# Kernel optimization log

Hardware: AMD Instinct MI355X
Metric: run time of the kernel (lower is better)

## Reference

```python
import jax, jax.numpy as jnp
import numpy as np

BATCH = 16384
IN_F = 768
OUT_F = 768
GRID_SIZE = 8           # act_fun.get_size()
GRID_LO, GRID_HI = -2.0, 2.0


def rbf_basis(x):
    """Gaussian RBF spline basis: [b, i] -> [b, a, i]."""
    grid = jnp.linspace(GRID_LO, GRID_HI, GRID_SIZE, dtype=x.dtype)  # [a]
    h = (GRID_HI - GRID_LO) / (GRID_SIZE - 1)
    z = (x[:, None, :] - grid[None, :, None]) / h                    # [b, a, i]
    return jnp.exp(-z * z)


def setup_inputs() -> dict:
    key = jax.random.key(0)
    k1, k2, k3 = jax.random.split(key, 3)
    x = jax.random.normal(k1, (BATCH, IN_F), dtype=jnp.float32)
    # xavier_normal_(gain=0.001): std = 0.001 * sqrt(2 / (fan_in + fan_out))
    std_wb = 0.001 * np.sqrt(2.0 / (IN_F + OUT_F))
    w_b = jax.random.normal(k2, (OUT_F, IN_F), dtype=jnp.float32) * std_wb
    w_s = jnp.ones((OUT_F, IN_F), dtype=jnp.float32)
    c = jax.random.normal(k3, (GRID_SIZE, OUT_F, IN_F), dtype=jnp.float32) * 0.001
    return {"x": x, "w_b": w_b, "w_s": w_s, "c": c}


def reference(x, w_b, w_s, c):
    # Original: sum_i[ (sum_a phi(x)_{bai} c_{aoi}) * w_s_{oi} + silu(x)_{bi} * w_b_{oi} ]
    phi = rbf_basis(x)                       # [b, a, i]
    cw = c * w_s[None, :, :]                 # fold scale into coeffs: [a, o, i]
    spline = jnp.einsum('bai,aoi->bo', phi, cw)   # fused contraction over (a, i)
    res = jax.nn.silu(x) @ w_b.T             # [b, o]
    return spline + res
```

## Files before the change

kernel.cpp:

```cpp
#include <hip/hip_runtime.h>
#include <hip/hip_bf16.h>

#define BATCH 16384
#define INF 768
#define OUTF 768
#define NSLAB 9
#define KTOT (NSLAB * INF)
#define BM 128
#define BN 128
#define BK 64
#define KB_TILES (INF / BK)
#define NIT (NSLAB * KB_TILES)

#define LOG2E 1.4426950408889634f
#define EXPM2 0.13533528323661270f

typedef __bf16 bf16x8 __attribute__((ext_vector_type(8)));
typedef float f32x4 __attribute__((ext_vector_type(4)));
typedef unsigned short ushort8v __attribute__((ext_vector_type(8)));

__device__ __forceinline__ unsigned short f2bf(float f) {
  unsigned u = __builtin_bit_cast(unsigned, f);
  u += 0x7fffu + ((u >> 16) & 1u);
  return (unsigned short)(u >> 16);
}

__device__ __forceinline__ unsigned cvt2(float a, float b) {
  __hip_bfloat162 h = __float22bfloat162_rn(make_float2(a, b));
  unsigned r;
  __builtin_memcpy(&r, &h, 4);
  return r;
}

__device__ __forceinline__ bf16x8 pack8(const f32x4 a, const f32x4 b) {
  union { uint4 u; bf16x8 v; } r;
  r.u.x = cvt2(a[0], a[1]); r.u.y = cvt2(a[2], a[3]);
  r.u.z = cvt2(b[0], b[1]); r.u.w = cvt2(b[2], b[3]);
  return r.v;
}

__device__ __forceinline__ void gload_lds16(const void* g, void* l) {
  __builtin_amdgcn_global_load_lds(
      (const __attribute__((address_space(1))) unsigned int*)g,
      (__attribute__((address_space(3))) unsigned int*)l, 16, 0, 0);
}

__global__ __launch_bounds__(256) void build_bext(
    const float* __restrict__ w_b, const float* __restrict__ w_s,
    const float* __restrict__ c, unsigned short* __restrict__ bext) {
  const int tid = blockIdx.x * 256 + threadIdx.x;
  const int o = tid / (KTOT / 8);
  const int k = (tid - o * (KTOT / 8)) * 8;
  const int a = k / INF;
  const int i = k - a * INF;
  float4 v0, v1;
  if (a < 8) {
    const float* cp = c + ((size_t)(a * OUTF + o)) * INF + i;
    const float* wp = w_s + (size_t)o * INF + i;
    const float4 c0 = *(const float4*)cp, c1 = *(const float4*)(cp + 4);
    const float4 s0 = *(const float4*)wp, s1 = *(const float4*)(wp + 4);
    v0 = make_float4(c0.x * s0.x, c0.y * s0.y, c0.z * s0.z, c0.w * s0.w);
    v1 = make_float4(c1.x * s1.x, c1.y * s1.y, c1.z * s1.z, c1.w * s1.w);
  } else {
    const float* bp = w_b + (size_t)o * INF + i;
    v0 = *(const float4*)bp;
    v1 = *(const float4*)(bp + 4);
  }
  ushort8v r;
  r[0] = f2bf(v0.x); r[1] = f2bf(v0.y); r[2] = f2bf(v0.z); r[3] = f2bf(v0.w);
  r[4] = f2bf(v1.x); r[5] = f2bf(v1.y); r[6] = f2bf(v1.z); r[7] = f2bf(v1.w);
  *(ushort8v*)(bext + (size_t)o * KTOT + k) = r;
}

__global__ __launch_bounds__(256, 2) void kan_gemm5(
    const float* __restrict__ x, const unsigned short* __restrict__ bext,
    float* __restrict__ out) {
  __shared__ unsigned short Bs[4][BN * BK];

  const int orig = blockIdx.x;
  const int bid = (orig & 7) * 96 + (orig >> 3);
  const int cb = bid / (BATCH / BM);
  const int rb = bid - cb * (BATCH / BM);
  const int row0 = rb * BM, col0 = cb * BN;

  const int t = threadIdx.x;
  const int lane = t & 63;
  const int w = t >> 6;
  const int lrow = lane & 15, lhi = lane >> 4;
  const int rgrp = lane >> 3, ch = lane & 7;

  f32x4 acc[2][8];
#pragma unroll
  for (int mt = 0; mt < 2; ++mt)
#pragma unroll
    for (int n = 0; n < 8; ++n)
      acc[mt][n] = (f32x4){0.f, 0.f, 0.f, 0.f};

  const unsigned short* gB0 =
      bext + (size_t)(col0 + w * 32 + rgrp) * KTOT + (size_t)(ch ^ rgrp) * 8;

  auto kt_of = [&](int k) {
    const int ib = k / 9;
    const int r = k - ib * 9;
    const int s = (r == 0) ? 8 : (r - 1);
    return s * KB_TILES + ib;
  };

  auto stage_b = [&](int k) {
    const unsigned short* gB = gB0 + (size_t)kt_of(k) * BK;
    unsigned short* l = &Bs[k & 3][w * 2048];
#pragma unroll
    for (int q = 0; q < 4; ++q)
      gload_lds16(gB + (size_t)q * 8 * KTOT, l + q * 512);
  };

  const float* xr0 = x + (size_t)(row0 + w * 32 + lrow) * INF;
  const float* xr1 = xr0 + 16 * INF;

  f32x4 ph[2][2][2], gg[2][2][2];
  f32x4 xn[2][2][2];

  auto load_x = [&](int ib) {
#pragma unroll
    for (int mt = 0; mt < 2; ++mt)
#pragma unroll
      for (int kk = 0; kk < 2; ++kk) {
        const float* p = (mt ? xr1 : xr0) + ib * BK + kk * 32 + lhi * 8;
        xn[mt][kk][0] = *(const f32x4*)p;
        xn[mt][kk][1] = *(const f32x4*)(p + 4);
      }
  };

  load_x(0);
  stage_b(0);
  stage_b(1);
  stage_b(2);
  asm volatile("s_waitcnt vmcnt(8)" ::: "memory");
  __builtin_amdgcn_s_barrier();
  __builtin_amdgcn_sched_barrier(0);

  int s_c = 8, ib_c = 0;
  for (int it = 0; it < NIT; ++it) {
    const int cur = it & 3;
    const bool xpf = (s_c == 6) && (ib_c + 1 < KB_TILES);
    if (xpf) load_x(ib_c + 1);
    if (it + 3 < NIT) stage_b(it + 3);

    bf16x8 af[2][2];
    if (s_c == 8) {
#pragma unroll
      for (int mt = 0; mt < 2; ++mt)
#pragma unroll
        for (int kk = 0; kk < 2; ++kk) {
          const f32x4 x0 = xn[mt][kk][0], x1 = xn[mt][kk][1];
          f32x4 s0, s1;
#pragma unroll
          for (int e = 0; e < 4; ++e) {
            s0[e] = x0[e] * __builtin_amdgcn_rcpf(
                        1.f + __builtin_amdgcn_exp2f(x0[e] * (-LOG2E)));
            s1[e] = x1[e] * __builtin_amdgcn_rcpf(
                        1.f + __builtin_amdgcn_exp2f(x1[e] * (-LOG2E)));
          }
          af[mt][kk] = pack8(s0, s1);
          const f32x4 z0 = x0 * 1.75f + 3.5f;
          const f32x4 z1 = x1 * 1.75f + 3.5f;
#pragma unroll
          for (int e = 0; e < 4; ++e) {
            ph[mt][kk][0][e] = __builtin_amdgcn_exp2f(-(z0[e] * z0[e]) * LOG2E);
            ph[mt][kk][1][e] = __builtin_amdgcn_exp2f(-(z1[e] * z1[e]) * LOG2E);
            gg[mt][kk][0][e] = __builtin_amdgcn_exp2f(z0[e] * (2.f * LOG2E) - LOG2E);
            gg[mt][kk][1][e] = __builtin_amdgcn_exp2f(z1[e] * (2.f * LOG2E) - LOG2E);
          }
        }
    } else {
#pragma unroll
      for (int mt = 0; mt < 2; ++mt)
#pragma unroll
        for (int kk = 0; kk < 2; ++kk) {
          af[mt][kk] = pack8(ph[mt][kk][0], ph[mt][kk][1]);
          ph[mt][kk][0] *= gg[mt][kk][0];
          ph[mt][kk][1] *= gg[mt][kk][1];
          gg[mt][kk][0] = gg[mt][kk][0] * EXPM2;
          gg[mt][kk][1] = gg[mt][kk][1] * EXPM2;
        }
    }

#pragma unroll
    for (int kk = 0; kk < 2; ++kk) {
      bf16x8 bfr[8];
#pragma unroll
      for (int n = 0; n < 8; ++n) {
        const int rowB = n * 16 + lrow;
        const int chB = (kk * 4 + lhi) ^ (lrow & 7);
        bfr[n] = *(const bf16x8*)&Bs[cur][rowB * 64 + chB * 8];
      }
#pragma unroll
      for (int mt = 0; mt < 2; ++mt)
#pragma unroll
        for (int n = 0; n < 8; ++n)
          acc[mt][n] = __builtin_amdgcn_mfma_f32_16x16x32_bf16(
              af[mt][kk], bfr[n], acc[mt][n], 0, 0, 0);
    }

    if (it < NIT - 3) {
      if (xpf) asm volatile("s_waitcnt vmcnt(16)" ::: "memory");
      else     asm volatile("s_waitcnt vmcnt(8)" ::: "memory");
    } else if (it == NIT - 3) {
      asm volatile("s_waitcnt vmcnt(4)" ::: "memory");
    } else if (it == NIT - 2) {
      asm volatile("s_waitcnt vmcnt(0)" ::: "memory");
    }
    if (it < NIT - 1) {
      __builtin_amdgcn_s_barrier();
      __builtin_amdgcn_sched_barrier(0);
    }

    if (s_c == 8)      { s_c = 0; }
    else if (s_c == 7) { s_c = 8; ib_c++; }
    else               { s_c++; }
  }

#pragma unroll
  for (int mt = 0; mt < 2; ++mt) {
#pragma unroll
    for (int n = 0; n < 8; ++n) {
      const int row = row0 + w * 32 + mt * 16 + lhi * 4;
      const int col = col0 + n * 16 + lrow;
#pragma unroll
      for (int r = 0; r < 4; ++r)
        out[(size_t)(row + r) * OUTF + col] = acc[mt][n][r];
    }
  }
}

#define PK (BK + 8)
__device__ __forceinline__ float phi_f(float x, float g) {
  float z = (x - g) * 1.75f;
  return __expf(-z * z);
}
__device__ __forceinline__ float silu_f(float x) {
  return x / (1.f + __expf(-x));
}

__global__ __launch_bounds__(256, 2) void kan_gemm_fb(
    const float* __restrict__ x, const float* __restrict__ w_b,
    const float* __restrict__ w_s, const float* __restrict__ c,
    float* __restrict__ out) {
  __shared__ unsigned short As[BM][PK];
  __shared__ unsigned short Bs[BN][PK];

  const int bid = blockIdx.x;
  const int cb = bid % (OUTF / BN);
  const int rb = bid / (OUTF / BN);
  const int row0 = rb * BM, col0 = cb * BN;

  const int t = threadIdx.x;
  const int lane = t & 63;
  const int w = t >> 6;
  const int wr = w >> 1, wc = w & 1;
  const int lrow = lane & 15, lhi = lane >> 4;

  f32x4 acc[4][4];
#pragma unroll
  for (int m = 0; m < 4; ++m)
#pragma unroll
    for (int n = 0; n < 4; ++n)
      acc[m][n] = (f32x4){0.f, 0.f, 0.f, 0.f};

  const int rsub = t >> 4;
  const int k4 = t & 15;

  for (int kt = 0; kt < KTOT / BK; ++kt) {
    const int a = kt / KB_TILES;
    const int i0 = (kt % KB_TILES) * BK;
    const float ga = -2.f + (float)a * (4.f / 7.f);

#pragma unroll
    for (int p = 0; p < 8; ++p) {
      const int r = p * 16 + rsub;
      const float4 xv = *(const float4*)(x + (size_t)(row0 + r) * INF + i0 + k4 * 4);
      ushort4 av;
      if (a < 8) {
        av.x = f2bf(phi_f(xv.x, ga)); av.y = f2bf(phi_f(xv.y, ga));
        av.z = f2bf(phi_f(xv.z, ga)); av.w = f2bf(phi_f(xv.w, ga));
      } else {
        av.x = f2bf(silu_f(xv.x)); av.y = f2bf(silu_f(xv.y));
        av.z = f2bf(silu_f(xv.z)); av.w = f2bf(silu_f(xv.w));
      }
      *(ushort4*)&As[r][k4 * 4] = av;

      ushort4 bv;
      if (a < 8) {
        const float4 cv = *(const float4*)(c + ((size_t)a * OUTF + col0 + r) * INF + i0 + k4 * 4);
        const float4 wv = *(const float4*)(w_s + (size_t)(col0 + r) * INF + i0 + k4 * 4);
        bv.x = f2bf(cv.x * wv.x); bv.y = f2bf(cv.y * wv.y);
        bv.z = f2bf(cv.z * wv.z); bv.w = f2bf(cv.w * wv.w);
      } else {
        const float4 bbv = *(const float4*)(w_b + (size_t)(col0 + r) * INF + i0 + k4 * 4);
        bv.x = f2bf(bbv.x); bv.y = f2bf(bbv.y);
        bv.z = f2bf(bbv.z); bv.w = f2bf(bbv.w);
      }
      *(ushort4*)&Bs[r][k4 * 4] = bv;
    }
    __syncthreads();

#pragma unroll
    for (int kk = 0; kk < 2; ++kk) {
      bf16x8 af[4], bfr[4];
#pragma unroll
      for (int m = 0; m < 4; ++m)
        af[m] = *(const bf16x8*)&As[wr * 64 + m * 16 + lrow][kk * 32 + lhi * 8];
#pragma unroll
      for (int n = 0; n < 4; ++n)
        bfr[n] = *(const bf16x8*)&Bs[wc * 64 + n * 16 + lrow][kk * 32 + lhi * 8];
#pragma unroll
      for (int m = 0; m < 4; ++m)
#pragma unroll
        for (int n = 0; n < 4; ++n)
          acc[m][n] = __builtin_amdgcn_mfma_f32_16x16x32_bf16(af[m], bfr[n], acc[m][n], 0, 0, 0);
    }
    __syncthreads();
  }

#pragma unroll
  for (int m = 0; m < 4; ++m) {
#pragma unroll
    for (int n = 0; n < 4; ++n) {
      const int row = row0 + wr * 64 + m * 16 + lhi * 4;
      const int col = col0 + wc * 64 + n * 16 + lrow;
#pragma unroll
      for (int r = 0; r < 4; ++r)
        out[(size_t)(row + r) * OUTF + col] = acc[m][n][r];
    }
  }
}

extern "C" void kernel_launch(void* const* d_in, const int* in_sizes, int n_in,
                              void* d_out, int out_size, void* d_ws, size_t ws_size,
                              hipStream_t stream) {
  const float* x   = (const float*)d_in[0];
  const float* w_b = (const float*)d_in[1];
  const float* w_s = (const float*)d_in[2];
  const float* c   = (const float*)d_in[3];
  float* out = (float*)d_out;

  const size_t need = (size_t)OUTF * KTOT * sizeof(unsigned short);
  if (ws_size >= need) {
    unsigned short* bext = (unsigned short*)d_ws;
    build_bext<<<(OUTF * KTOT / 8) / 256, 256, 0, stream>>>(w_b, w_s, c, bext);
    kan_gemm5<<<(BATCH / BM) * (OUTF / BN), 256, 0, stream>>>(x, bext, out);
  } else {
    kan_gemm_fb<<<(BATCH / BM) * (OUTF / BN), 256, 0, stream>>>(x, w_b, w_s, c, out);
  }
}
```

Baseline: 246.6 us.

## Retile KAN GEMM to 64x128x32 blocks with column-split warps

Shrinks the block tile to 64 rows by 128 columns with a K step of 32, and reassigns warps so each owns 32 output columns across all 64 rows. The B staging, swizzle, x prefetch and waitcnt schedule are adjusted to match, and the block-index remap is updated for the doubled grid. The intent is more blocks and smaller per-iteration work for better latency hiding and balance. The cost is that every warp recomputes the RBF/SiLU basis for the same rows, and twice as many barrier-separated iterations run with fewer MFMAs each.

```diff
diff --git a/kernel.cpp b/kernel.cpp
--- a/kernel.cpp
+++ b/kernel.cpp
@@ -6,9 +6,9 @@
 #define OUTF 768
 #define NSLAB 9
 #define KTOT (NSLAB * INF)
-#define BM 128
+#define BM 64
 #define BN 128
-#define BK 64
+#define BK 32
 #define KB_TILES (INF / BK)
 #define NIT (NSLAB * KB_TILES)
 
@@ -72,13 +72,13 @@
   *(ushort8v*)(bext + (size_t)o * KTOT + k) = r;
 }
 
-__global__ __launch_bounds__(256, 2) void kan_gemm5(
+__global__ __launch_bounds__(256, 2) void kan_gemm6(
     const float* __restrict__ x, const unsigned short* __restrict__ bext,
     float* __restrict__ out) {
   __shared__ unsigned short Bs[4][BN * BK];
 
   const int orig = blockIdx.x;
-  const int bid = (orig & 7) * 96 + (orig >> 3);
+  const int bid = (orig & 7) * 192 + (orig >> 3);
   const int cb = bid / (BATCH / BM);
   const int rb = bid - cb * (BATCH / BM);
   const int row0 = rb * BM, col0 = cb * BN;
@@ -87,128 +87,108 @@
   const int lane = t & 63;
   const int w = t >> 6;
   const int lrow = lane & 15, lhi = lane >> 4;
-  const int rgrp = lane >> 3, ch = lane & 7;
-
-  f32x4 acc[2][8];
-#pragma unroll
-  for (int mt = 0; mt < 2; ++mt)
-#pragma unroll
-    for (int n = 0; n < 8; ++n)
+
+  f32x4 acc[4][2];
+#pragma unroll
+  for (int mt = 0; mt < 4; ++mt)
+#pragma unroll
+    for (int n = 0; n < 2; ++n)
       acc[mt][n] = (f32x4){0.f, 0.f, 0.f, 0.f};
 
-  const unsigned short* gB0 =
-      bext + (size_t)(col0 + w * 32 + rgrp) * KTOT + (size_t)(ch ^ rgrp) * 8;
-
-  auto kt_of = [&](int k) {
-    const int ib = k / 9;
-    const int r = k - ib * 9;
-    const int s = (r == 0) ? 8 : (r - 1);
-    return s * KB_TILES + ib;
+  const int srow = t >> 2;
+  const int sch = (t & 3) ^ (srow & 3);
+  const unsigned short* gS0 = bext + (size_t)(col0 + srow) * KTOT + sch * 8;
+  const unsigned short* gS1 = gS0 + (size_t)64 * KTOT;
+
+  auto stage_b = [&](int k) {
+    const int ib = k / 9, r = k - ib * 9;
+    const int kt = (r ? r - 1 : 8) * KB_TILES + ib;
+    unsigned short* l = &Bs[k & 3][t * 8];
+    gload_lds16(gS0 + (size_t)kt * BK, l);
+    gload_lds16(gS1 + (size_t)kt * BK, l + 2048);
   };
 
-  auto stage_b = [&](int k) {
-    const unsigned short* gB = gB0 + (size_t)kt_of(k) * BK;
-    unsigned short* l = &Bs[k & 3][w * 2048];
-#pragma unroll
-    for (int q = 0; q < 4; ++q)
-      gload_lds16(gB + (size_t)q * 8 * KTOT, l + q * 512);
-  };
-
-  const float* xr0 = x + (size_t)(row0 + w * 32 + lrow) * INF;
-  const float* xr1 = xr0 + 16 * INF;
-
-  f32x4 ph[2][2][2], gg[2][2][2];
-  f32x4 xn[2][2][2];
+  f32x4 ph[4][2], gg[4][2];
+  f32x4 xn[4][2];
 
   auto load_x = [&](int ib) {
 #pragma unroll
-    for (int mt = 0; mt < 2; ++mt)
-#pragma unroll
-      for (int kk = 0; kk < 2; ++kk) {
-        const float* p = (mt ? xr1 : xr0) + ib * BK + kk * 32 + lhi * 8;
-        xn[mt][kk][0] = *(const f32x4*)p;
-        xn[mt][kk][1] = *(const f32x4*)(p + 4);
-      }
+    for (int mt = 0; mt < 4; ++mt) {
+      const float* p = x + (size_t)(row0 + mt * 16 + lrow) * INF + ib * BK + lhi * 8;
+      xn[mt][0] = *(const f32x4*)p;
+      xn[mt][1] = *(const f32x4*)(p + 4);
+    }
   };
 
   load_x(0);
   stage_b(0);
   stage_b(1);
   stage_b(2);
-  asm volatile("s_waitcnt vmcnt(8)" ::: "memory");
+  asm volatile("s_waitcnt vmcnt(4)" ::: "memory");
   __builtin_amdgcn_s_barrier();
   __builtin_amdgcn_sched_barrier(0);
 
   int s_c = 8, ib_c = 0;
   for (int it = 0; it < NIT; ++it) {
     const int cur = it & 3;
-    const bool xpf = (s_c == 6) && (ib_c + 1 < KB_TILES);
+    const bool xpf = (s_c == 7) && (ib_c + 1 < KB_TILES);
     if (xpf) load_x(ib_c + 1);
     if (it + 3 < NIT) stage_b(it + 3);
 
-    bf16x8 af[2][2];
+    bf16x8 af[4];
     if (s_c == 8) {
 #pragma unroll
-      for (int mt = 0; mt < 2; ++mt)
-#pragma unroll
-        for (int kk = 0; kk < 2; ++kk) {
-          const f32x4 x0 = xn[mt][kk][0], x1 = xn[mt][kk][1];
-          f32x4 s0, s1;
-#pragma unroll
-          for (int e = 0; e < 4; ++e) {
-            s0[e] = x0[e] * __builtin_amdgcn_rcpf(
-                        1.f + __builtin_amdgcn_exp2f(x0[e] * (-LOG2E)));
-            s1[e] = x1[e] * __builtin_amdgcn_rcpf(
-                        1.f + __builtin_amdgcn_exp2f(x1[e] * (-LOG2E)));
-          }
-          af[mt][kk] = pack8(s0, s1);
-          const f32x4 z0 = x0 * 1.75f + 3.5f;
-          const f32x4 z1 = x1 * 1.75f + 3.5f;
-#pragma unroll
-          for (int e = 0; e < 4; ++e) {
-            ph[mt][kk][0][e] = __builtin_amdgcn_exp2f(-(z0[e] * z0[e]) * LOG2E);
-            ph[mt][kk][1][e] = __builtin_amdgcn_exp2f(-(z1[e] * z1[e]) * LOG2E);
-            gg[mt][kk][0][e] = __builtin_amdgcn_exp2f(z0[e] * (2.f * LOG2E) - LOG2E);
-            gg[mt][kk][1][e] = __builtin_amdgcn_exp2f(z1[e] * (2.f * LOG2E) - LOG2E);
-          }
+      for (int mt = 0; mt < 4; ++mt) {
+        const f32x4 x0 = xn[mt][0], x1 = xn[mt][1];
+        f32x4 s0, s1;
+#pragma unroll
+        for (int e = 0; e < 4; ++e) {
+          s0[e] = x0[e] * __builtin_amdgcn_rcpf(
+                      1.f + __builtin_amdgcn_exp2f(x0[e] * (-LOG2E)));
+          s1[e] = x1[e] * __builtin_amdgcn_rcpf(
+                      1.f + __builtin_amdgcn_exp2f(x1[e] * (-LOG2E)));
         }
+        af[mt] = pack8(s0, s1);
+        const f32x4 z0 = x0 * 1.75f + 3.5f;
+        const f32x4 z1 = x1 * 1.75f + 3.5f;
+#pragma unroll
+        for (int e = 0; e < 4; ++e) {
+          ph[mt][0][e] = __builtin_amdgcn_exp2f(-(z0[e] * z0[e]) * LOG2E);
+          ph[mt][1][e] = __builtin_amdgcn_exp2f(-(z1[e] * z1[e]) * LOG2E);
+          gg[mt][0][e] = __builtin_amdgcn_exp2f(z0[e] * (2.f * LOG2E) - LOG2E);
+          gg[mt][1][e] = __builtin_amdgcn_exp2f(z1[e] * (2.f * LOG2E) - LOG2E);
+        }
+      }
     } else {
 #pragma unroll
-      for (int mt = 0; mt < 2; ++mt)
-#pragma unroll
-        for (int kk = 0; kk < 2; ++kk) {
-          af[mt][kk] = pack8(ph[mt][kk][0], ph[mt][kk][1]);
-          ph[mt][kk][0] *= gg[mt][kk][0];
-          ph[mt][kk][1] *= gg[mt][kk][1];
-          gg[mt][kk][0] = gg[mt][kk][0] * EXPM2;
-          gg[mt][kk][1] = gg[mt][kk][1] * EXPM2;
-        }
-    }
-
-#pragma unroll
-    for (int kk = 0; kk < 2; ++kk) {
-      bf16x8 bfr[8];
-#pragma unroll
-      for (int n = 0; n < 8; ++n) {
-        const int rowB = n * 16 + lrow;
-        const int chB = (kk * 4 + lhi) ^ (lrow & 7);
-        bfr[n] = *(const bf16x8*)&Bs[cur][rowB * 64 + chB * 8];
+      for (int mt = 0; mt < 4; ++mt) {
+        af[mt] = pack8(ph[mt][0], ph[mt][1]);
+        ph[mt][0] *= gg[mt][0];
+        ph[mt][1] *= gg[mt][1];
+        gg[mt][0] = gg[mt][0] * EXPM2;
+        gg[mt][1] = gg[mt][1] * EXPM2;
       }
-#pragma unroll
-      for (int mt = 0; mt < 2; ++mt)
-#pragma unroll
-        for (int n = 0; n < 8; ++n)
-          acc[mt][n] = __builtin_amdgcn_mfma_f32_16x16x32_bf16(
-              af[mt][kk], bfr[n], acc[mt][n], 0, 0, 0);
-    }
-
-    if (it < NIT - 3) {
-      if (xpf) asm volatile("s_waitcnt vmcnt(16)" ::: "memory");
-      else     asm volatile("s_waitcnt vmcnt(8)" ::: "memory");
+    }
+
+    bf16x8 bfr[2];
+    const int chB = lhi ^ (lrow & 3);
+#pragma unroll
+    for (int n = 0; n < 2; ++n)
+      bfr[n] = *(const bf16x8*)&Bs[cur][(w * 32 + n * 16 + lrow) * 32 + chB * 8];
+#pragma unroll
+    for (int mt = 0; mt < 4; ++mt)
+#pragma unroll
+      for (int n = 0; n < 2; ++n)
+        acc[mt][n] = __builtin_amdgcn_mfma_f32_16x16x32_bf16(
+            af[mt], bfr[n], acc[mt][n], 0, 0, 0);
+
+    if (it == NIT - 2) {
+      asm volatile("s_waitcnt vmcnt(0)" ::: "memory");
     } else if (it == NIT - 3) {
-      asm volatile("s_waitcnt vmcnt(4)" ::: "memory");
-    } else if (it == NIT - 2) {
-      asm volatile("s_waitcnt vmcnt(0)" ::: "memory");
+      asm volatile("s_waitcnt vmcnt(2)" ::: "memory");
+    } else if (it < NIT - 3) {
+      if (xpf) asm volatile("s_waitcnt vmcnt(2)" ::: "memory");
+      else     asm volatile("s_waitcnt vmcnt(4)" ::: "memory");
     }
     if (it < NIT - 1) {
       __builtin_amdgcn_s_barrier();
@@ -221,11 +201,11 @@
   }
 
 #pragma unroll
-  for (int mt = 0; mt < 2; ++mt) {
-#pragma unroll
-    for (int n = 0; n < 8; ++n) {
-      const int row = row0 + w * 32 + mt * 16 + lhi * 4;
-      const int col = col0 + n * 16 + lrow;
+  for (int mt = 0; mt < 4; ++mt) {
+#pragma unroll
+    for (int n = 0; n < 2; ++n) {
+      const int row = row0 + mt * 16 + lhi * 4;
+      const int col = col0 + w * 32 + n * 16 + lrow;
 #pragma unroll
       for (int r = 0; r < 4; ++r)
         out[(size_t)(row + r) * OUTF + col] = acc[mt][n][r];
@@ -233,7 +213,6 @@
   }
 }
 
-#define PK (BK + 8)
 __device__ __forceinline__ float phi_f(float x, float g) {
   float z = (x - g) * 1.75f;
   return __expf(-z * z);
@@ -246,13 +225,13 @@
     const float* __restrict__ x, const float* __restrict__ w_b,
     const float* __restrict__ w_s, const float* __restrict__ c,
     float* __restrict__ out) {
-  __shared__ unsigned short As[BM][PK];
-  __shared__ unsigned short Bs[BN][PK];
+  __shared__ unsigned short As[128][72];
+  __shared__ unsigned short Bs[128][72];
 
   const int bid = blockIdx.x;
-  const int cb = bid % (OUTF / BN);
-  const int rb = bid / (OUTF / BN);
-  const int row0 = rb * BM, col0 = cb * BN;
+  const int cb = bid % (OUTF / 128);
+  const int rb = bid / (OUTF / 128);
+  const int row0 = rb * 128, col0 = cb * 128;
 
   const int t = threadIdx.x;
   const int lane = t & 63;
@@ -270,9 +249,9 @@
   const int rsub = t >> 4;
   const int k4 = t & 15;
 
-  for (int kt = 0; kt < KTOT / BK; ++kt) {
-    const int a = kt / KB_TILES;
-    const int i0 = (kt % KB_TILES) * BK;
+  for (int kt = 0; kt < KTOT / 64; ++kt) {
+    const int a = kt / (INF / 64);
+    const int i0 = (kt % (INF / 64)) * 64;
     const float ga = -2.f + (float)a * (4.f / 7.f);
 
 #pragma unroll
@@ -348,8 +327,8 @@
   if (ws_size >= need) {
     unsigned short* bext = (unsigned short*)d_ws;
     build_bext<<<(OUTF * KTOT / 8) / 256, 256, 0, stream>>>(w_b, w_s, c, bext);
-    kan_gemm5<<<(BATCH / BM) * (OUTF / BN), 256, 0, stream>>>(x, bext, out);
+    kan_gemm6<<<(BATCH / BM) * (OUTF / BN), 256, 0, stream>>>(x, bext, out);
   } else {
-    kan_gemm_fb<<<(BATCH / BM) * (OUTF / BN), 256, 0, stream>>>(x, w_b, w_s, c, out);
-  }
-}
+    kan_gemm_fb<<<(BATCH / 128) * (OUTF / 128), 256, 0, stream>>>(x, w_b, w_s, c, out);
+  }
+}
```

Measured after the change: 604.4 us. +145.1%, slower.

## Pre-tile B into contiguous swizzled tiles and triple-buffer with 3 blocks/CU

Applied to the files above, without the earlier changes.

The weight-prep kernel now writes B in a tile-contiguous, pre-swizzled order so each stage is a straight contiguous copy into LDS instead of strided row reads. The main GEMM drops from four to three LDS buffers so three blocks fit per CU, and the loop is restructured as 12 outer input tiles by 9 unrolled slab steps with x loaded directly at slab start instead of prefetched. Fewer buffers mean a shorter prefetch distance and more exposed latency, and the register cap at 3 blocks/CU may force spills.

```diff
diff --git a/kernel.cpp b/kernel.cpp
--- a/kernel.cpp
+++ b/kernel.cpp
@@ -9,11 +9,15 @@
 #define BM 128
 #define BN 128
 #define BK 64
-#define KB_TILES (INF / BK)
-#define NIT (NSLAB * KB_TILES)
+#define KB_TILES 12
+#define NTILES (NSLAB * KB_TILES)
 
 #define LOG2E 1.4426950408889634f
 #define EXPM2 0.13533528323661270f
+
+#define TILE_SH 8192
+#define IB_SH   8192
+#define SLAB_SH (KB_TILES * TILE_SH)
 
 typedef __bf16 bf16x8 __attribute__((ext_vector_type(8)));
 typedef float f32x4 __attribute__((ext_vector_type(4)));
@@ -45,14 +49,22 @@
       (__attribute__((address_space(3))) unsigned int*)l, 16, 0, 0);
 }
 
-__global__ __launch_bounds__(256) void build_bext(
+__global__ __launch_bounds__(256) void build_bext2(
     const float* __restrict__ w_b, const float* __restrict__ w_s,
-    const float* __restrict__ c, unsigned short* __restrict__ bext) {
-  const int tid = blockIdx.x * 256 + threadIdx.x;
-  const int o = tid / (KTOT / 8);
-  const int k = (tid - o * (KTOT / 8)) * 8;
-  const int a = k / INF;
-  const int i = k - a * INF;
+    const float* __restrict__ c, unsigned short* __restrict__ bt) {
+  const int gid = blockIdx.x * 256 + threadIdx.x;
+  const int lane = gid & 63;
+  const int q = (gid >> 6) & 3;
+  const int wv = (gid >> 8) & 3;
+  const int tile = gid >> 10;
+  const int kt = tile % NTILES;
+  const int cbq = tile / NTILES;
+  const int a = kt / KB_TILES;
+  const int ib = kt - a * KB_TILES;
+  const int rg = lane >> 3, chh = lane & 7;
+  const int o = cbq * 128 + wv * 32 + q * 8 + rg;
+  const int i = ib * 64 + (chh ^ rg) * 8;
+
   float4 v0, v1;
   if (a < 8) {
     const float* cp = c + ((size_t)(a * OUTF + o)) * INF + i;
@@ -69,13 +81,13 @@
   ushort8v r;
   r[0] = f2bf(v0.x); r[1] = f2bf(v0.y); r[2] = f2bf(v0.z); r[3] = f2bf(v0.w);
   r[4] = f2bf(v1.x); r[5] = f2bf(v1.y); r[6] = f2bf(v1.z); r[7] = f2bf(v1.w);
-  *(ushort8v*)(bext + (size_t)o * KTOT + k) = r;
-}
-
-__global__ __launch_bounds__(256, 2) void kan_gemm5(
-    const float* __restrict__ x, const unsigned short* __restrict__ bext,
+  *(ushort8v*)(bt + (size_t)gid * 8) = r;
+}
+
+__global__ __launch_bounds__(256, 3) void kan_gemm7(
+    const float* __restrict__ x, const unsigned short* __restrict__ bt,
     float* __restrict__ out) {
-  __shared__ unsigned short Bs[4][BN * BK];
+  __shared__ unsigned short Bs[3][BN * BK];
 
   const int orig = blockIdx.x;
   const int bid = (orig & 7) * 96 + (orig >> 3);
@@ -87,7 +99,6 @@
   const int lane = t & 63;
   const int w = t >> 6;
   const int lrow = lane & 15, lhi = lane >> 4;
-  const int rgrp = lane >> 3, ch = lane & 7;
 
   f32x4 acc[2][8];
 #pragma unroll
@@ -96,128 +107,117 @@
     for (int n = 0; n < 8; ++n)
       acc[mt][n] = (f32x4){0.f, 0.f, 0.f, 0.f};
 
-  const unsigned short* gB0 =
-      bext + (size_t)(col0 + w * 32 + rgrp) * KTOT + (size_t)(ch ^ rgrp) * 8;
-
-  auto kt_of = [&](int k) {
-    const int ib = k / 9;
-    const int r = k - ib * 9;
-    const int s = (r == 0) ? 8 : (r - 1);
-    return s * KB_TILES + ib;
+  const unsigned short* gt =
+      bt + (size_t)cb * NTILES * TILE_SH + w * 2048 + lane * 8;
+  const float* xb = x + (size_t)(row0 + w * 32 + lrow) * INF;
+
+  const int c0 = lhi ^ (lrow & 7);
+  const int c1 = (4 + lhi) ^ (lrow & 7);
+  const unsigned short* pB0 = &Bs[0][lrow * 64 + c0 * 8];
+  const unsigned short* pB1 = &Bs[0][lrow * 64 + c1 * 8];
+
+  f32x4 ph[2][2][2], gg[2][2][2];
+
+  auto stage = [&](const unsigned short* src, int slot) {
+#pragma unroll
+    for (int q = 0; q < 4; ++q)
+      gload_lds16(src + q * 512, &Bs[slot][w * 2048 + q * 512]);
   };
 
-  auto stage_b = [&](int k) {
-    const unsigned short* gB = gB0 + (size_t)kt_of(k) * BK;
-    unsigned short* l = &Bs[k & 3][w * 2048];
-#pragma unroll
-    for (int q = 0; q < 4; ++q)
-      gload_lds16(gB + (size_t)q * 8 * KTOT, l + q * 512);
+  auto mma_kk = [&](int kk, int slot, bf16x8 af0, bf16x8 af1) {
+    const unsigned short* pB = kk ? pB1 : pB0;
+#pragma unroll
+    for (int n = 0; n < 8; ++n) {
+      const bf16x8 b = *(const bf16x8*)(pB + slot * TILE_SH + n * 1024);
+      acc[0][n] = __builtin_amdgcn_mfma_f32_16x16x32_bf16(af0, b, acc[0][n], 0, 0, 0);
+      acc[1][n] = __builtin_amdgcn_mfma_f32_16x16x32_bf16(af1, b, acc[1][n], 0, 0, 0);
+    }
   };
 
-  const float* xr0 = x + (size_t)(row0 + w * 32 + lrow) * INF;
-  const float* xr1 = xr0 + 16 * INF;
-
-  f32x4 ph[2][2][2], gg[2][2][2];
-  f32x4 xn[2][2][2];
-
-  auto load_x = [&](int ib) {
-#pragma unroll
-    for (int mt = 0; mt < 2; ++mt)
-#pragma unroll
-      for (int kk = 0; kk < 2; ++kk) {
-        const float* p = (mt ? xr1 : xr0) + ib * BK + kk * 32 + lhi * 8;
-        xn[mt][kk][0] = *(const f32x4*)p;
-        xn[mt][kk][1] = *(const f32x4*)(p + 4);
-      }
-  };
-
-  load_x(0);
-  stage_b(0);
-  stage_b(1);
-  stage_b(2);
-  asm volatile("s_waitcnt vmcnt(8)" ::: "memory");
+  const unsigned short* gib = gt;
+  stage(gib + 8 * SLAB_SH, 0);
+  stage(gib, 1);
+  asm volatile("s_waitcnt vmcnt(4)" ::: "memory");
   __builtin_amdgcn_s_barrier();
   __builtin_amdgcn_sched_barrier(0);
 
-  int s_c = 8, ib_c = 0;
-  for (int it = 0; it < NIT; ++it) {
-    const int cur = it & 3;
-    const bool xpf = (s_c == 6) && (ib_c + 1 < KB_TILES);
-    if (xpf) load_x(ib_c + 1);
-    if (it + 3 < NIT) stage_b(it + 3);
-
-    bf16x8 af[2][2];
-    if (s_c == 8) {
-#pragma unroll
-      for (int mt = 0; mt < 2; ++mt)
+#pragma clang loop unroll(disable)
+  for (int ib = 0; ib < KB_TILES; ++ib) {
+    const float* xib = xb + ib * BK;
+    const bool last = (ib == KB_TILES - 1);
+#pragma unroll
+    for (int j = 0; j < 9; ++j) {
+      const int slot = j % 3;
+
+      if (j == 0) {
+        f32x4 xr[4][2];
+#pragma unroll
+        for (int g = 0; g < 4; ++g) {
+          const float* p = xib + (g >> 1) * 16 * INF + (g & 1) * 32 + lhi * 8;
+          xr[g][0] = *(const f32x4*)p;
+          xr[g][1] = *(const f32x4*)(p + 4);
+        }
+        stage(gib + 1 * SLAB_SH, 2);
 #pragma unroll
         for (int kk = 0; kk < 2; ++kk) {
-          const f32x4 x0 = xn[mt][kk][0], x1 = xn[mt][kk][1];
-          f32x4 s0, s1;
-#pragma unroll
-          for (int e = 0; e < 4; ++e) {
-            s0[e] = x0[e] * __builtin_amdgcn_rcpf(
-                        1.f + __builtin_amdgcn_exp2f(x0[e] * (-LOG2E)));
-            s1[e] = x1[e] * __builtin_amdgcn_rcpf(
-                        1.f + __builtin_amdgcn_exp2f(x1[e] * (-LOG2E)));
+          bf16x8 af[2];
+#pragma unroll
+          for (int mt = 0; mt < 2; ++mt) {
+            const f32x4 x0 = xr[mt * 2 + kk][0], x1 = xr[mt * 2 + kk][1];
+            f32x4 s0, s1;
+#pragma unroll
+            for (int e = 0; e < 4; ++e) {
+              s0[e] = x0[e] * __builtin_amdgcn_rcpf(
+                          1.f + __builtin_amdgcn_exp2f(x0[e] * (-LOG2E)));
+              s1[e] = x1[e] * __builtin_amdgcn_rcpf(
+                          1.f + __builtin_amdgcn_exp2f(x1[e] * (-LOG2E)));
+            }
+            af[mt] = pack8(s0, s1);
+            const f32x4 z0 = x0 * 1.75f + 3.5f;
+            const f32x4 z1 = x1 * 1.75f + 3.5f;
+#pragma unroll
+            for (int e = 0; e < 4; ++e) {
+              ph[mt][kk][0][e] = __builtin_amdgcn_exp2f(-(z0[e] * z0[e]) * LOG2E);
+              ph[mt][kk][1][e] = __builtin_amdgcn_exp2f(-(z1[e] * z1[e]) * LOG2E);
+              gg[mt][kk][0][e] = __builtin_amdgcn_exp2f(z0[e] * (2.f * LOG2E) - LOG2E);
+              gg[mt][kk][1][e] = __builtin_amdgcn_exp2f(z1[e] * (2.f * LOG2E) - LOG2E);
+            }
           }
-          af[mt][kk] = pack8(s0, s1);
-          const f32x4 z0 = x0 * 1.75f + 3.5f;
-          const f32x4 z1 = x1 * 1.75f + 3.5f;
-#pragma unroll
-          for (int e = 0; e < 4; ++e) {
-            ph[mt][kk][0][e] = __builtin_amdgcn_exp2f(-(z0[e] * z0[e]) * LOG2E);
-            ph[mt][kk][1][e] = __builtin_amdgcn_exp2f(-(z1[e] * z1[e]) * LOG2E);
-            gg[mt][kk][0][e] = __builtin_amdgcn_exp2f(z0[e] * (2.f * LOG2E) - LOG2E);
-            gg[mt][kk][1][e] = __builtin_amdgcn_exp2f(z1[e] * (2.f * LOG2E) - LOG2E);
+          mma_kk(kk, 0, af[0], af[1]);
+        }
+      } else {
+        if (j <= 6) {
+          stage(gib + (j + 1) * SLAB_SH, (j + 2) % 3);
+        } else if (!last) {
+          if (j == 7) stage(gib + 8 * SLAB_SH + IB_SH, 0);
+          else        stage(gib + IB_SH, 1);
+        }
+#pragma unroll
+        for (int kk = 0; kk < 2; ++kk) {
+          bf16x8 af[2];
+#pragma unroll
+          for (int mt = 0; mt < 2; ++mt) {
+            af[mt] = pack8(ph[mt][kk][0], ph[mt][kk][1]);
+            ph[mt][kk][0] *= gg[mt][kk][0];
+            ph[mt][kk][1] *= gg[mt][kk][1];
+            gg[mt][kk][0] = gg[mt][kk][0] * EXPM2;
+            gg[mt][kk][1] = gg[mt][kk][1] * EXPM2;
           }
+          mma_kk(kk, slot, af[0], af[1]);
         }
-    } else {
-#pragma unroll
-      for (int mt = 0; mt < 2; ++mt)
-#pragma unroll
-        for (int kk = 0; kk < 2; ++kk) {
-          af[mt][kk] = pack8(ph[mt][kk][0], ph[mt][kk][1]);
-          ph[mt][kk][0] *= gg[mt][kk][0];
-          ph[mt][kk][1] *= gg[mt][kk][1];
-          gg[mt][kk][0] = gg[mt][kk][0] * EXPM2;
-          gg[mt][kk][1] = gg[mt][kk][1] * EXPM2;
-        }
-    }
-
-#pragma unroll
-    for (int kk = 0; kk < 2; ++kk) {
-      bf16x8 bfr[8];
-#pragma unroll
-      for (int n = 0; n < 8; ++n) {
-        const int rowB = n * 16 + lrow;
-        const int chB = (kk * 4 + lhi) ^ (lrow & 7);
-        bfr[n] = *(const bf16x8*)&Bs[cur][rowB * 64 + chB * 8];
-      }
-#pragma unroll
-      for (int mt = 0; mt < 2; ++mt)
-#pragma unroll
-        for (int n = 0; n < 8; ++n)
-          acc[mt][n] = __builtin_amdgcn_mfma_f32_16x16x32_bf16(
-              af[mt][kk], bfr[n], acc[mt][n], 0, 0, 0);
-    }
-
-    if (it < NIT - 3) {
-      if (xpf) asm volatile("s_waitcnt vmcnt(16)" ::: "memory");
-      else     asm volatile("s_waitcnt vmcnt(8)" ::: "memory");
-    } else if (it == NIT - 3) {
-      asm volatile("s_waitcnt vmcnt(4)" ::: "memory");
-    } else if (it == NIT - 2) {
-      asm volatile("s_waitcnt vmcnt(0)" ::: "memory");
-    }
-    if (it < NIT - 1) {
-      __builtin_amdgcn_s_barrier();
-      __builtin_amdgcn_sched_barrier(0);
-    }
-
-    if (s_c == 8)      { s_c = 0; }
-    else if (s_c == 7) { s_c = 8; ib_c++; }
-    else               { s_c++; }
+      }
+
+      if (!last || j < 7) {
+        asm volatile("s_waitcnt vmcnt(4)" ::: "memory");
+      } else if (j == 7) {
+        asm volatile("s_waitcnt vmcnt(0)" ::: "memory");
+      }
+      if (!(last && j == 8)) {
+        __builtin_amdgcn_s_barrier();
+        __builtin_amdgcn_sched_barrier(0);
+      }
+    }
+    gib += IB_SH;
   }
 
 #pragma unroll
@@ -233,7 +233,6 @@
   }
 }
 
-#define PK (BK + 8)
 __device__ __forceinline__ float phi_f(float x, float g) {
   float z = (x - g) * 1.75f;
   return __expf(-z * z);
@@ -246,13 +245,13 @@
     const float* __restrict__ x, const float* __restrict__ w_b,
     const float* __restrict__ w_s, const float* __restrict__ c,
     float* __restrict__ out) {
-  __shared__ unsigned short As[BM][PK];
-  __shared__ unsigned short Bs[BN][PK];
+  __shared__ unsigned short As[128][72];
+  __shared__ unsigned short Bs[128][72];
 
   const int bid = blockIdx.x;
-  const int cb = bid % (OUTF / BN);
-  const int rb = bid / (OUTF / BN);
-  const int row0 = rb * BM, col0 = cb * BN;
+  const int cbf = bid % (OUTF / 128);
+  const int rbf = bid / (OUTF / 128);
+  const int row0 = rbf * 128, col0 = cbf * 128;
 
   const int t = threadIdx.x;
   const int lane = t & 63;
@@ -270,9 +269,9 @@
   const int rsub = t >> 4;
   const int k4 = t & 15;
 
-  for (int kt = 0; kt < KTOT / BK; ++kt) {
-    const int a = kt / KB_TILES;
-    const int i0 = (kt % KB_TILES) * BK;
+  for (int kt = 0; kt < KTOT / 64; ++kt) {
+    const int a = kt / (INF / 64);
+    const int i0 = (kt % (INF / 64)) * 64;
     const float ga = -2.f + (float)a * (4.f / 7.f);
 
 #pragma unroll
@@ -346,10 +345,10 @@
 
   const size_t need = (size_t)OUTF * KTOT * sizeof(unsigned short);
   if (ws_size >= need) {
-    unsigned short* bext = (unsigned short*)d_ws;
-    build_bext<<<(OUTF * KTOT / 8) / 256, 256, 0, stream>>>(w_b, w_s, c, bext);
-    kan_gemm5<<<(BATCH / BM) * (OUTF / BN), 256, 0, stream>>>(x, bext, out);
+    unsigned short* bt = (unsigned short*)d_ws;
+    build_bext2<<<(OUTF * KTOT / 8) / 256, 256, 0, stream>>>(w_b, w_s, c, bt);
+    kan_gemm7<<<(BATCH / BM) * (OUTF / BN), 256, 0, stream>>>(x, bt, out);
   } else {
-    kan_gemm_fb<<<(BATCH / BM) * (OUTF / BN), 256, 0, stream>>>(x, w_b, w_s, c, out);
-  }
-}
+    kan_gemm_fb<<<(BATCH / 128) * (OUTF / 128), 256, 0, stream>>>(x, w_b, w_s, c, out);
+  }
+}
```

Measured after the change: 326.6 us. 32.5% more time.
